# Kernel tuning notes

Measured on AMD Instinct MI355X. Metric: run time of the kernel, lower is better.

Reference implementation:

```python
import jax, jax.numpy as jnp
import numpy as np

COORD_W, WIDTH_W, VALID_W = 5.0, 1.0, 1.0  # module init defaults
COST_COORD_W, COST_WIDTH_W = 5.0, 1.0      # hardcoded in compute_cost_matrix


def _hungarian(cost):
    """Pure-numpy linear_sum_assignment (Jonker-Volgenant style, e-maxx variant).
    cost: [R, C] float. Returns (row_ind, col_ind) matching scipy semantics
    (min(R, C) pairs minimizing total cost)."""
    cost = np.asarray(cost, dtype=np.float64)
    transposed = cost.shape[0] > cost.shape[1]
    C = cost.T if transposed else cost
    n, m = C.shape  # n <= m
    u = np.zeros(n + 1)
    v = np.zeros(m + 1)
    p = np.zeros(m + 1, dtype=np.int64)   # p[j] = 1-indexed row assigned to col j
    way = np.zeros(m + 1, dtype=np.int64)
    for i in range(1, n + 1):
        p[0] = i
        j0 = 0
        minv = np.full(m + 1, np.inf)
        used = np.zeros(m + 1, dtype=bool)
        while True:
            used[j0] = True
            i0 = p[j0]
            jf = np.nonzero(~used[1:])[0] + 1  # free columns (1-indexed)
            cur = C[i0 - 1, jf - 1] - u[i0] - v[jf]
            upd = cur < minv[jf]
            minv[jf] = np.where(upd, cur, minv[jf])
            way[jf[upd]] = j0
            j1 = jf[np.argmin(minv[jf])]
            delta = minv[j1]
            u[p[used]] += delta
            v[used] -= delta
            minv[jf] -= delta
            j0 = j1
            if p[j0] == 0:
                break
        while j0:
            j1 = way[j0]
            p[j0] = p[j1]
            j0 = j1
    col4row = np.zeros(n, dtype=np.int64)
    for j in range(1, m + 1):
        if p[j] > 0:
            col4row[p[j] - 1] = j - 1
    rows = np.arange(n, dtype=np.int64)
    return (col4row, rows) if transposed else (rows, col4row)


def _compute_matching(pred_strokes, targets):
    """Per-batch Hungarian matching on the (detached) cost matrix.
    Returns padded pred idx P [B,S], gt idx G [B,S], match mask M [B,S], num_gt N [B]."""
    ps = np.asarray(pred_strokes)
    tg = np.asarray(targets)
    B, S, _ = ps.shape
    P = np.zeros((B, S), dtype=np.int64)
    G = np.zeros((B, S), dtype=np.int64)
    M = np.zeros((B, S), dtype=np.float32)
    N = np.zeros((B,), dtype=np.float32)
    for b in range(B):
        valid = np.nonzero(tg[b, :, 10] > 0.5)[0]
        ng = len(valid)
        N[b] = ng
        if ng == 0:
            continue
        gt = tg[b, valid, :10]                      # [ng, 10]
        d = np.abs(ps[b, :, None, :] - gt[None])    # [S, ng, 10]
        cost = COST_COORD_W * d[..., :8].sum(-1) + COST_WIDTH_W * d[..., 8:10].sum(-1)
        pi, gi = _hungarian(cost)
        P[b, :ng] = pi
        G[b, :ng] = valid[gi]
        M[b, :ng] = 1.0
    return P, G, M, N


def _loss(pred_strokes, pred_validity, targets, P, G, M, N):
    gt_strokes = targets[..., :10]
    gt_val = targets[..., 10:11]
    mp = jnp.take_along_axis(pred_strokes, P[..., None], axis=1)  # [B,S,10]
    mg = jnp.take_along_axis(gt_strokes, G[..., None], axis=1)    # [B,S,10]
    ad = jnp.abs(mp - mg) * M[..., None]
    ng = jnp.maximum(N, 1.0)
    coord = ad[..., :8].sum(axis=(1, 2)) / (ng * 8.0)             # per-batch L1 mean
    width = ad[..., 8:10].sum(axis=(1, 2)) / (ng * 2.0)
    # BCE with torch-style log clamp at -100
    logp = jnp.clip(jnp.log(pred_validity), -100.0)
    log1p = jnp.clip(jnp.log(1.0 - pred_validity), -100.0)
    bce = (-(gt_val * logp + (1.0 - gt_val) * log1p)).mean(axis=(1, 2))
    loss_b = jnp.where(N > 0, COORD_W * coord + WIDTH_W * width + VALID_W * bce, bce)
    return loss_b.mean()


def setup_inputs() -> dict:
    key = jax.random.key(0)
    k1, k2, k3 = jax.random.split(key, 3)
    B, S = 256, 64
    return {
        "pred_strokes": jax.random.uniform(k1, (B, S, 10), dtype=jnp.float32),
        "pred_validity": jax.random.uniform(k2, (B, S, 1), dtype=jnp.float32),
        "targets": jax.random.uniform(k3, (B, S, 11), dtype=jnp.float32),
    }


def reference(pred_strokes, pred_validity, targets):
    P, G, M, N = _compute_matching(pred_strokes, targets)
    return _loss(pred_strokes, pred_validity, targets,
                 jnp.asarray(P), jnp.asarray(G), jnp.asarray(M), jnp.asarray(N))
```

## Files before the change

kernel.cpp:

```cpp
#include <hip/hip_runtime.h>
#include <math.h>


#define SS 64
#define LDS_FENCE() asm volatile("s_waitcnt lgkmcnt(0)" ::: "memory")

__device__ __forceinline__ int rlane_i(int x, int lane) {
    return __builtin_amdgcn_readlane(x, lane);
}
__device__ __forceinline__ double rlane_d(double x, int lane) {
    return __hiloint2double(rlane_i(__double2hiint(x), lane),
                            rlane_i(__double2loint(x), lane));
}

template<int CTRL>
__device__ __forceinline__ unsigned dpp_shift_ff(unsigned x) {
    return (unsigned)__builtin_amdgcn_update_dpp(
        (int)0xFFFFFFFFu, (int)x, CTRL, 0xF, 0xF, false);
}
__device__ __forceinline__ unsigned wave_min_u32_to63(unsigned x) {
    unsigned y;
    y = dpp_shift_ff<0x111>(x); x = x < y ? x : y;
    y = dpp_shift_ff<0x112>(x); x = x < y ? x : y;
    y = dpp_shift_ff<0x114>(x); x = x < y ? x : y;
    y = dpp_shift_ff<0x118>(x); x = x < y ? x : y;
    y = dpp_shift_ff<0x142>(x); x = x < y ? x : y;
    y = dpp_shift_ff<0x143>(x); x = x < y ? x : y;
    return x;
}

__global__ __launch_bounds__(64) void detr_match_loss_kernel(
    const float* __restrict__ pred_strokes,
    const float* __restrict__ pred_validity,
    const float* __restrict__ targets,
    double* __restrict__ loss_ws)
{
    const int b = blockIdx.x;
    const int t = threadIdx.x;
    const float* ps = pred_strokes  + (size_t)b * SS * 10;
    const float* pv = pred_validity + (size_t)b * SS;
    const float* tg = targets      + (size_t)b * SS * 11;

    __shared__ float  Cs[SS * SS];
    __shared__ float  tgs[SS * 11];
    __shared__ int    vidx[SS];
    __shared__ int    col4row[SS];

#pragma unroll
    for (int k = 0; k < 11; ++k) tgs[k * SS + t] = tg[k * SS + t];
    LDS_FENCE();

    const float gv    = tgs[t * 11 + 10];
    const bool  valid = gv > 0.5f;
    const unsigned long long vmask = __ballot(valid);
    const int ng = __popcll(vmask);
    if (valid) {
        const int rank = __popcll(vmask & ((1ull << t) - 1ull));
        vidx[rank] = t;
    }
    LDS_FENCE();

    double bterm;
    {
        const float pvv = pv[t];
        const float lp  = fmaxf(logf(pvv), -100.0f);
        const float l1p = fmaxf(logf(1.0f - pvv), -100.0f);
        bterm = -((double)gv * (double)lp + (double)(1.0f - gv) * (double)l1p);
    }

    double csum = 0.0, wsum = 0.0;

    if (ng > 0) {
        float pr[10];
#pragma unroll
        for (int k = 0; k < 10; ++k) pr[k] = ps[t * 10 + k];

        double u_reg = 0.0;
        int    p_j   = 0;
        unsigned long long colclaim = 0ull;
        unsigned long long freerows = 0ull;

        for (int i = 0; i < ng; ++i) {
            const float* g = &tgs[vidx[i] * 11];
            float d[10];
#pragma unroll
            for (int k = 0; k < 10; ++k) d[k] = fabsf(pr[k] - g[k]);
            const float cs = ((d[0] + d[1]) + (d[2] + d[3]))
                           + ((d[4] + d[5]) + (d[6] + d[7]));
            const float wd = d[8] + d[9];
            float c;
            {
#pragma clang fp contract(off)
                c = 5.0f * cs + wd;
            }
            Cs[i * SS + t] = c;

            const unsigned key = __float_as_uint(c);
            const unsigned kr  = wave_min_u32_to63(key);
            const unsigned mst = (unsigned)rlane_i((int)kr, 63);
            const unsigned long long rbal = __ballot(key == mst);
            const int jstar = __ffsll(rbal) - 1;
            if (t == i) u_reg = (double)__uint_as_float(mst);
            if (!((colclaim >> jstar) & 1ull)) {
                colclaim |= 1ull << jstar;
                if (t == jstar) p_j = i + 1;
            } else {
                freerows |= 1ull << i;
            }
        }

        double v_j = 0.0;

        while (freerows) {
            const int r0 = __ffsll(freerows) - 1;
            freerows &= freerows - 1;
            const int i = r0 + 1;

            double minv_j   = __builtin_inf();
            int    way_j    = 0;
            bool   used_j   = false;
            bool   row_used = (t == r0);
            double u0       = rlane_d(u_reg, r0);
            int    j0       = 0;
            float  Cval     = Cs[r0 * SS + t];

            for (;;) {
                used_j = used_j || (t + 1 == j0);
                const double cur = ((double)Cval - u0) - v_j;
                if (!used_j && cur < minv_j) { minv_j = cur; way_j = j0; }

                const unsigned hraw = (unsigned)__double2hiint(minv_j);
                const bool     mneg = (hraw & 0x80000000u) != 0;
                const unsigned key  = used_j ? 0xFFFFFFFFu
                                    : (mneg ? ~hraw : (hraw | 0x80000000u));
                const unsigned kr    = wave_min_u32_to63(key);
                const unsigned hstar = (unsigned)rlane_i((int)kr, 63);
                unsigned long long bal = __ballot(key == hstar);
                int j1 = __ffsll(bal);
                int i1 = rlane_i(p_j, j1 - 1);

                float C_next = 0.0f;
                if (i1 != 0) C_next = Cs[(i1 - 1) * SS + t];

                if (__popcll(bal) > 1) {
                    const unsigned lraw = (unsigned)__double2loint(minv_j);
                    const unsigned lo   = (key == hstar)
                                        ? (mneg ? ~lraw : lraw) : 0xFFFFFFFFu;
                    const unsigned lr    = wave_min_u32_to63(lo);
                    const unsigned lstar = (unsigned)rlane_i((int)lr, 63);
                    bal = __ballot(key == hstar && lo == lstar);
                    j1  = __ffsll(bal);
                    i1  = rlane_i(p_j, j1 - 1);
                    if (i1 != 0) C_next = Cs[(i1 - 1) * SS + t];
                }

                const double delta  = rlane_d(minv_j, j1 - 1);
                const double u_next = (i1 != 0) ? rlane_d(u_reg, i1 - 1) : 0.0;

                if (row_used) u_reg += delta;
                if (used_j)   v_j   -= delta;
                else          minv_j -= delta;
                row_used = row_used || (t == i1 - 1);

                j0 = j1;
                if (i1 == 0) break;
                u0 = u_next; Cval = C_next;
            }

            int jj = j0;
            while (jj != 0) {
                const int jp   = rlane_i(way_j, jj - 1);
                const int pnew = (jp == 0) ? i : rlane_i(p_j, jp - 1);
                if (t == jj - 1) p_j = pnew;
                jj = jp;
            }
        }

        if (p_j > 0) col4row[p_j - 1] = t;
        LDS_FENCE();

        if (t < ng) {
            const float* g  = &tgs[vidx[t] * 11];
            const float* mp = ps + col4row[t] * 10;
#pragma unroll
            for (int k = 0; k < 8; ++k) csum += (double)fabsf(mp[k] - g[k]);
            wsum = (double)fabsf(mp[8] - g[8]) + (double)fabsf(mp[9] - g[9]);
        }
    }

    double s0 = csum, s1 = wsum, s2 = bterm;
#pragma unroll
    for (int off = 1; off < 64; off <<= 1) {
        s0 += __shfl_xor(s0, off, 64);
        s1 += __shfl_xor(s1, off, 64);
        s2 += __shfl_xor(s2, off, 64);
    }
    if (t == 0) {
        const double bce = s2 / 64.0;
        const double loss = (ng > 0)
            ? 5.0 * (s0 / ((double)ng * 8.0)) + (s1 / ((double)ng * 2.0)) + bce
            : bce;
        loss_ws[b] = loss;
    }
}

__global__ __launch_bounds__(256) void detr_reduce_kernel(
    const double* __restrict__ ws, float* __restrict__ out, int B)
{
    const int t = threadIdx.x;
    double x = 0.0;
    for (int idx = t; idx < B; idx += 256) x += ws[idx];
    for (int off = 1; off < 64; off <<= 1) x += __shfl_xor(x, off, 64);
    __shared__ double part[4];
    if ((t & 63) == 0) part[t >> 6] = x;
    __syncthreads();
    if (t == 0) {
        double s = part[0] + part[1] + part[2] + part[3];
        out[0] = (float)(s / (double)B);
    }
}

extern "C" void kernel_launch(void* const* d_in, const int* in_sizes, int n_in,
                              void* d_out, int out_size, void* d_ws, size_t ws_size,
                              hipStream_t stream) {
    const float* ps = (const float*)d_in[0];
    const float* pv = (const float*)d_in[1];
    const float* tg = (const float*)d_in[2];
    float* out = (float*)d_out;
    double* ws = (double*)d_ws;
    const int B = in_sizes[0] / (SS * 10);

    detr_match_loss_kernel<<<B, SS, 0, stream>>>(ps, pv, tg, ws);
    detr_reduce_kernel<<<1, 256, 0, stream>>>(ws, out, B);
}
```

Baseline: 84.55 us.

## Fuse final reduction via last-block atomic counter and trim Hungarian inner loop

The separate reduction kernel is replaced by a last-block-done pattern: each block stores its loss with release semantics, bumps an atomic counter, and the final block sums all per-batch losses. Target rows now stay in registers and are broadcast with readlane instead of being staged in LDS with a valid-index table. The cost matrix is stored as double so the inner loop skips conversions. The next free row's cost is prefetched, and delta is rebuilt from the reduced high word plus one readlane instead of two. This adds a memset launch, doubles LDS use, and changes the DPP min step to fill lanes with their own value.

New measurement: 87.11 us. 1.03x slower.

```diff
diff --git a/kernel.cpp b/kernel.cpp
--- a/kernel.cpp
+++ b/kernel.cpp
@@ -14,18 +14,18 @@
 }
 
 template<int CTRL>
-__device__ __forceinline__ unsigned dpp_shift_ff(unsigned x) {
-    return (unsigned)__builtin_amdgcn_update_dpp(
-        (int)0xFFFFFFFFu, (int)x, CTRL, 0xF, 0xF, false);
+__device__ __forceinline__ unsigned mstep(unsigned x) {
+    const unsigned y = (unsigned)__builtin_amdgcn_update_dpp(
+        (int)x, (int)x, CTRL, 0xF, 0xF, false);
+    return x < y ? x : y;
 }
 __device__ __forceinline__ unsigned wave_min_u32_to63(unsigned x) {
-    unsigned y;
-    y = dpp_shift_ff<0x111>(x); x = x < y ? x : y;
-    y = dpp_shift_ff<0x112>(x); x = x < y ? x : y;
-    y = dpp_shift_ff<0x114>(x); x = x < y ? x : y;
-    y = dpp_shift_ff<0x118>(x); x = x < y ? x : y;
-    y = dpp_shift_ff<0x142>(x); x = x < y ? x : y;
-    y = dpp_shift_ff<0x143>(x); x = x < y ? x : y;
+    x = mstep<0x111>(x);
+    x = mstep<0x112>(x);
+    x = mstep<0x114>(x);
+    x = mstep<0x118>(x);
+    x = mstep<0x142>(x);
+    x = mstep<0x143>(x);
     return x;
 }
 
@@ -33,7 +33,9 @@
     const float* __restrict__ pred_strokes,
     const float* __restrict__ pred_validity,
     const float* __restrict__ targets,
-    double* __restrict__ loss_ws)
+    double* __restrict__ loss_ws,
+    unsigned* __restrict__ counter,
+    float* __restrict__ out, int B)
 {
     const int b = blockIdx.x;
     const int t = threadIdx.x;
@@ -41,24 +43,16 @@
     const float* pv = pred_validity + (size_t)b * SS;
     const float* tg = targets      + (size_t)b * SS * 11;
 
-    __shared__ float  Cs[SS * SS];
-    __shared__ float  tgs[SS * 11];
-    __shared__ int    vidx[SS];
+    __shared__ double Cs[SS * SS];
     __shared__ int    col4row[SS];
 
-#pragma unroll
-    for (int k = 0; k < 11; ++k) tgs[k * SS + t] = tg[k * SS + t];
-    LDS_FENCE();
-
-    const float gv    = tgs[t * 11 + 10];
+    float tgv[11];
+#pragma unroll
+    for (int k = 0; k < 11; ++k) tgv[k] = tg[t * 11 + k];
+    const float gv    = tgv[10];
     const bool  valid = gv > 0.5f;
     const unsigned long long vmask = __ballot(valid);
     const int ng = __popcll(vmask);
-    if (valid) {
-        const int rank = __popcll(vmask & ((1ull << t) - 1ull));
-        vidx[rank] = t;
-    }
-    LDS_FENCE();
 
     double bterm;
     {
@@ -79,9 +73,16 @@
         int    p_j   = 0;
         unsigned long long colclaim = 0ull;
         unsigned long long freerows = 0ull;
+        unsigned long long vm = vmask;
 
         for (int i = 0; i < ng; ++i) {
-            const float* g = &tgs[vidx[i] * 11];
+            const int vrow = __ffsll(vm) - 1;
+            vm &= vm - 1;
+            float g[10];
+#pragma unroll
+            for (int k = 0; k < 10; ++k)
+                g[k] = __uint_as_float(
+                    (unsigned)rlane_i(__float_as_int(tgv[k]), vrow));
             float d[10];
 #pragma unroll
             for (int k = 0; k < 10; ++k) d[k] = fabsf(pr[k] - g[k]);
@@ -93,11 +94,11 @@
 #pragma clang fp contract(off)
                 c = 5.0f * cs + wd;
             }
-            Cs[i * SS + t] = c;
+            Cs[i * SS + t] = (double)c;
 
             const unsigned key = __float_as_uint(c);
-            const unsigned kr  = wave_min_u32_to63(key);
-            const unsigned mst = (unsigned)rlane_i((int)kr, 63);
+            const unsigned mst = (unsigned)rlane_i(
+                (int)wave_min_u32_to63(key), 63);
             const unsigned long long rbal = __ballot(key == mst);
             const int jstar = __ffsll(rbal) - 1;
             if (t == i) u_reg = (double)__uint_as_float(mst);
@@ -110,10 +111,13 @@
         }
 
         double v_j = 0.0;
+        int nr0 = freerows ? (__ffsll(freerows) - 1) : -1;
+        double Chead = (nr0 >= 0) ? Cs[nr0 * SS + t] : 0.0;
 
         while (freerows) {
-            const int r0 = __ffsll(freerows) - 1;
+            const int r0 = nr0;
             freerows &= freerows - 1;
+            nr0 = freerows ? (__ffsll(freerows) - 1) : -1;
             const int i = r0 + 1;
 
             double minv_j   = __builtin_inf();
@@ -122,39 +126,44 @@
             bool   row_used = (t == r0);
             double u0       = rlane_d(u_reg, r0);
             int    j0       = 0;
-            float  Cval     = Cs[r0 * SS + t];
+            double Cval     = Chead;
+
+            const double Chead_next = (nr0 >= 0) ? Cs[nr0 * SS + t] : 0.0;
 
             for (;;) {
                 used_j = used_j || (t + 1 == j0);
-                const double cur = ((double)Cval - u0) - v_j;
+                const double cur = (Cval - u0) - v_j;
                 if (!used_j && cur < minv_j) { minv_j = cur; way_j = j0; }
 
-                const unsigned hraw = (unsigned)__double2hiint(minv_j);
-                const bool     mneg = (hraw & 0x80000000u) != 0;
-                const unsigned key  = used_j ? 0xFFFFFFFFu
-                                    : (mneg ? ~hraw : (hraw | 0x80000000u));
-                const unsigned kr    = wave_min_u32_to63(key);
-                const unsigned hstar = (unsigned)rlane_i((int)kr, 63);
+                const int      hi  = __double2hiint(minv_j);
+                const int      s31 = hi >> 31;
+                unsigned key = (unsigned)(hi ^ (s31 | (int)0x80000000));
+                if (used_j) key = 0xFFFFFFFFu;
+                const unsigned hstar = (unsigned)rlane_i(
+                    (int)wave_min_u32_to63(key), 63);
                 unsigned long long bal = __ballot(key == hstar);
                 int j1 = __ffsll(bal);
                 int i1 = rlane_i(p_j, j1 - 1);
 
-                float C_next = 0.0f;
+                double C_next = 0.0;
                 if (i1 != 0) C_next = Cs[(i1 - 1) * SS + t];
 
                 if (__popcll(bal) > 1) {
                     const unsigned lraw = (unsigned)__double2loint(minv_j);
                     const unsigned lo   = (key == hstar)
-                                        ? (mneg ? ~lraw : lraw) : 0xFFFFFFFFu;
-                    const unsigned lr    = wave_min_u32_to63(lo);
-                    const unsigned lstar = (unsigned)rlane_i((int)lr, 63);
+                                        ? (s31 ? ~lraw : lraw) : 0xFFFFFFFFu;
+                    const unsigned lstar = (unsigned)rlane_i(
+                        (int)wave_min_u32_to63(lo), 63);
                     bal = __ballot(key == hstar && lo == lstar);
                     j1  = __ffsll(bal);
                     i1  = rlane_i(p_j, j1 - 1);
                     if (i1 != 0) C_next = Cs[(i1 - 1) * SS + t];
                 }
 
-                const double delta  = rlane_d(minv_j, j1 - 1);
+                const int hmin = (hstar & 0x80000000u)
+                               ? (int)(hstar & 0x7FFFFFFFu) : (int)~hstar;
+                const int lmin = rlane_i(__double2loint(minv_j), j1 - 1);
+                const double delta  = __hiloint2double(hmin, lmin);
                 const double u_next = (i1 != 0) ? rlane_d(u_reg, i1 - 1) : 0.0;
 
                 if (row_used) u_reg += delta;
@@ -174,17 +183,18 @@
                 if (t == jj - 1) p_j = pnew;
                 jj = jp;
             }
+            Chead = Chead_next;
         }
 
         if (p_j > 0) col4row[p_j - 1] = t;
         LDS_FENCE();
 
-        if (t < ng) {
-            const float* g  = &tgs[vidx[t] * 11];
-            const float* mp = ps + col4row[t] * 10;
-#pragma unroll
-            for (int k = 0; k < 8; ++k) csum += (double)fabsf(mp[k] - g[k]);
-            wsum = (double)fabsf(mp[8] - g[8]) + (double)fabsf(mp[9] - g[9]);
+        if (valid) {
+            const int r = __popcll(vmask & ((1ull << t) - 1ull));
+            const float* mp = ps + col4row[r] * 10;
+#pragma unroll
+            for (int k = 0; k < 8; ++k) csum += (double)fabsf(mp[k] - tgv[k]);
+            wsum = (double)fabsf(mp[8] - tgv[8]) + (double)fabsf(mp[9] - tgv[9]);
         }
     }
 
@@ -195,28 +205,28 @@
         s1 += __shfl_xor(s1, off, 64);
         s2 += __shfl_xor(s2, off, 64);
     }
+
+    unsigned prev = 0;
     if (t == 0) {
         const double bce = s2 / 64.0;
         const double loss = (ng > 0)
             ? 5.0 * (s0 / ((double)ng * 8.0)) + (s1 / ((double)ng * 2.0)) + bce
             : bce;
-        loss_ws[b] = loss;
-    }
-}
-
-__global__ __launch_bounds__(256) void detr_reduce_kernel(
-    const double* __restrict__ ws, float* __restrict__ out, int B)
-{
-    const int t = threadIdx.x;
-    double x = 0.0;
-    for (int idx = t; idx < B; idx += 256) x += ws[idx];
-    for (int off = 1; off < 64; off <<= 1) x += __shfl_xor(x, off, 64);
-    __shared__ double part[4];
-    if ((t & 63) == 0) part[t >> 6] = x;
-    __syncthreads();
-    if (t == 0) {
-        double s = part[0] + part[1] + part[2] + part[3];
-        out[0] = (float)(s / (double)B);
+        __hip_atomic_store(&loss_ws[b], loss,
+                           __ATOMIC_RELEASE, __HIP_MEMORY_SCOPE_AGENT);
+        prev = __hip_atomic_fetch_add(counter, 1u,
+                                      __ATOMIC_ACQ_REL, __HIP_MEMORY_SCOPE_AGENT);
+    }
+    prev = (unsigned)rlane_i((int)prev, 0);
+
+    if (prev == (unsigned)(B - 1)) {
+        double x = 0.0;
+        for (int idx = t; idx < B; idx += SS)
+            x += __hip_atomic_load(&loss_ws[idx],
+                                   __ATOMIC_RELAXED, __HIP_MEMORY_SCOPE_AGENT);
+#pragma unroll
+        for (int off = 1; off < 64; off <<= 1) x += __shfl_xor(x, off, 64);
+        if (t == 0) out[0] = (float)(x / (double)B);
     }
 }
 
@@ -227,9 +237,11 @@
     const float* pv = (const float*)d_in[1];
     const float* tg = (const float*)d_in[2];
     float* out = (float*)d_out;
-    double* ws = (double*)d_ws;
     const int B = in_sizes[0] / (SS * 10);
 
-    detr_match_loss_kernel<<<B, SS, 0, stream>>>(ps, pv, tg, ws);
-    detr_reduce_kernel<<<1, 256, 0, stream>>>(ws, out, B);
-}
+    double*   ws  = (double*)d_ws;
+    unsigned* cnt = (unsigned*)((char*)d_ws + (size_t)B * sizeof(double));
+    hipMemsetAsync(cnt, 0, sizeof(unsigned), stream);
+
+    detr_match_loss_kernel<<<B, SS, 0, stream>>>(ps, pv, tg, ws, cnt, out, B);
+}
```
